# Optimization experiments

Measured on AMD Instinct MI355X. Metric: run time of the kernel, lower is better.

Reference implementation:

```python
import jax, jax.numpy as jnp
import numpy as np

T, B, V, LMAX = 512, 32, 4096, 32
NEG = -1e30  # log-domain 'zero'


def setup_inputs() -> dict:
    key = jax.random.key(0)
    k1, k2, k3, k4 = jax.random.split(key, 4)
    acts = jax.random.normal(k1, (T, B, V), dtype=jnp.float32)  # pre-softmax logits
    label_lens = jax.random.randint(k2, (B,), 16, LMAX + 1)
    act_lens = jax.random.randint(k3, (B,), T // 2, T + 1)
    total = int(jnp.sum(label_lens))
    labels = jax.random.randint(k4, (total,), 1, V)  # flat concat; blank=0 excluded
    return {"acts": acts, "labels": labels, "act_lens": act_lens, "label_lens": label_lens}


def _ctc_total_loss(acts, labels, act_lens, label_lens):
    # warp-ctc semantics: acts are logits; softmax applied internally; blank index = 0.
    logp = jax.nn.log_softmax(acts, axis=-1)  # (T, B, V)

    # Unpack flat concatenated labels into padded (B, LMAX).
    offsets = jnp.cumsum(label_lens) - label_lens
    pos = jnp.arange(LMAX)
    idx = jnp.clip(offsets[:, None] + pos[None, :], 0, labels.shape[0] - 1)
    lab = jnp.where(pos[None, :] < label_lens[:, None], labels[idx], 0)  # (B, LMAX)

    # Extended label sequence with interleaved blanks: S = 2*LMAX + 1.
    S = 2 * LMAX + 1
    ext = jnp.zeros((B, S), dtype=labels.dtype).at[:, 1::2].set(lab)
    s_idx = jnp.arange(S)
    s_valid = s_idx[None, :] < (2 * label_lens + 1)[:, None]  # (B, S)
    ext_m2 = jnp.concatenate([jnp.zeros((B, 2), ext.dtype), ext[:, :-2]], axis=1)
    can_skip = (ext != 0) & (ext != ext_m2) & (s_idx[None, :] >= 2)  # (B, S)

    # Pre-gather emissions along the lattice: (T, B, S).
    emit = jnp.take_along_axis(logp, ext[None, :, :], axis=2)

    alpha0 = jnp.where(s_idx[None, :] <= 1, emit[0], NEG)
    alpha0 = jnp.where(s_valid, alpha0, NEG)

    def step(alpha, xs):
        emit_t, t = xs
        a1 = jnp.concatenate([jnp.full((B, 1), NEG, alpha.dtype), alpha[:, :-1]], axis=1)
        a2 = jnp.concatenate([jnp.full((B, 2), NEG, alpha.dtype), alpha[:, :-2]], axis=1)
        a2 = jnp.where(can_skip, a2, NEG)
        m = jnp.maximum(alpha, jnp.maximum(a1, a2))
        new = m + jnp.log(jnp.exp(alpha - m) + jnp.exp(a1 - m) + jnp.exp(a2 - m)) + emit_t
        new = jnp.where(s_valid, new, NEG)
        # Freeze alpha once past each example's act_len (ragged time lengths).
        alpha = jnp.where((t < act_lens)[:, None], new, alpha)
        return alpha, None

    ts = jnp.arange(1, T)
    alpha, _ = jax.lax.scan(step, alpha0, (emit[1:], ts))

    end = 2 * label_lens  # final blank state per example
    l1 = jnp.take_along_axis(alpha, end[:, None], axis=1)[:, 0]
    l2 = jnp.take_along_axis(alpha, jnp.clip(end - 1, 0, S - 1)[:, None], axis=1)[:, 0]
    loss = -jnp.logaddexp(l1, l2)  # per-example NLL
    # size_average=False, length_average=False: return summed cost, shape (1,)
    return jnp.sum(loss)[None]


def reference(acts, labels, act_lens, label_lens):
    return _ctc_total_loss(acts, labels, act_lens, label_lens)
```

## Files before the change

### kernel.cpp

```cpp
#include <hip/hip_runtime.h>
#include <hip/hip_bf16.h>
#include <math.h>

#define T_DIM 512
#define B_DIM 32
#define V_DIM 4096
#define LMAX 32
#define S_DIM 65
#define NEG (-1e30f)
#define EROWS 528
#define LOG2E 1.4426950408889634f
#define LN2   0.6931471805599453f

__device__ __forceinline__ float fexp2(float x) {
#if __has_builtin(__builtin_amdgcn_exp2f)
    return __builtin_amdgcn_exp2f(x);
#else
    return exp2f(x);
#endif
}
__device__ __forceinline__ float flog2(float x) {
#if __has_builtin(__builtin_amdgcn_logf)
    return __builtin_amdgcn_logf(x);
#else
    return log2f(x);
#endif
}
__device__ __forceinline__ float gload(const float* p) {
    return *(const __attribute__((address_space(1))) float*)((unsigned long long)p);
}
__device__ __forceinline__ float lse2_2(float x, float y) {
    float m = fmaxf(x, y);
    return m + flog2(fexp2(x - m) + fexp2(y - m));
}
__device__ __forceinline__ float lse3_2(float x, float y, float z) {
    float m = fmaxf(x, fmaxf(y, z));
    return m + flog2(fexp2(x - m) + fexp2(y - m) + fexp2(z - m));
}

__global__ void k_ext(const int* __restrict__ labels,
                      const int* __restrict__ label_lens,
                      int total,
                      int* __restrict__ ext,
                      int* __restrict__ canskip) {
    int idx = blockIdx.x * blockDim.x + threadIdx.x;
    if (idx >= B_DIM * S_DIM) return;
    int b = idx / S_DIM;
    int s = idx % S_DIM;
    int off = 0;
    for (int i = 0; i < b; ++i) off += label_lens[i];
    int len = label_lens[b];

    auto getext = [&](int ss) -> int {
        if ((ss & 1) == 0) return 0;
        int j = ss >> 1;
        if (j >= len) return 0;
        int id = off + j;
        if (id > total - 1) id = total - 1;
        if (id < 0) id = 0;
        return labels[id];
    };

    int e = getext(s);
    ext[idx] = e;
    int cs = 0;
    if (s >= 2) {
        int em2 = getext(s - 2);
        cs = (e != 0 && e != em2) ? 1 : 0;
    }
    canskip[idx] = cs;
}

__global__ __launch_bounds__(256) void k_logz_emit(const float* __restrict__ acts,
                                                   const int* __restrict__ ext,
                                                   float* __restrict__ emitA,
                                                   float* __restrict__ emit64) {
    int bid = blockIdx.x;
    int t = bid / B_DIM;
    int b = bid % B_DIM;
    const float* row = acts + (size_t)bid * V_DIM;
    int tid = threadIdx.x;

    const float4* row4 = reinterpret_cast<const float4*>(row);
    float4 v[4];
#pragma unroll
    for (int k = 0; k < 4; ++k) v[k] = row4[tid + k * 256];

    float mx = -INFINITY;
#pragma unroll
    for (int k = 0; k < 4; ++k)
        mx = fmaxf(mx, fmaxf(fmaxf(v[k].x, v[k].y), fmaxf(v[k].z, v[k].w)));
#pragma unroll
    for (int off = 32; off > 0; off >>= 1) mx = fmaxf(mx, __shfl_xor(mx, off));

    __shared__ float smax[4], ssum[4];
    int wave = tid >> 6, lane = tid & 63;
    if (lane == 0) smax[wave] = mx;
    __syncthreads();
    mx = fmaxf(fmaxf(smax[0], smax[1]), fmaxf(smax[2], smax[3]));

    float mxL = mx * LOG2E;
    float s = 0.f;
#pragma unroll
    for (int k = 0; k < 4; ++k) {
        s += fexp2(fmaf(v[k].x, LOG2E, -mxL));
        s += fexp2(fmaf(v[k].y, LOG2E, -mxL));
        s += fexp2(fmaf(v[k].z, LOG2E, -mxL));
        s += fexp2(fmaf(v[k].w, LOG2E, -mxL));
    }
#pragma unroll
    for (int off = 32; off > 0; off >>= 1) s += __shfl_xor(s, off);
    if (lane == 0) ssum[wave] = s;
    __syncthreads();
    s = ssum[0] + ssum[1] + ssum[2] + ssum[3];

    float logZ2 = mxL + flog2(s);

    if (tid < 64) {
        int lab = ext[b * S_DIM + tid];
        emitA[((size_t)b * EROWS + t) * 64 + tid] = fmaf(row[lab], LOG2E, -logZ2);
    } else if (tid == 64) {
        emit64[(size_t)b * EROWS + t] = fmaf(row[0], LOG2E, -logZ2);
    }
}

__global__ __launch_bounds__(64) void k_forward(const float* __restrict__ emitA,
                                                const float* __restrict__ emit64,
                                                const int* __restrict__ canskip,
                                                const int* __restrict__ act_lens,
                                                const int* __restrict__ label_lens,
                                                float* __restrict__ losses) {
    int b = blockIdx.x;
    int l = threadIdx.x;
    int len = label_lens[b];
    int alen = act_lens[b];
    int Svalid = 2 * len + 1;
    bool validS  = l < Svalid;
    bool validM1 = (l >= 1) && (l - 1 < Svalid);
    bool validM2 = (l >= 2) && (l - 2 < Svalid);
    const int* csb = canskip + b * S_DIM;
    bool skipS  = csb[l] != 0;
    bool skipM1 = (l >= 1) ? (csb[l - 1] != 0) : false;
    bool skipM2 = (l >= 2) ? (csb[l - 2] != 0) : false;

    const float* pb  = emitA + (size_t)b * EROWS * 64;
    const float* p64 = emit64 + (size_t)b * EROWS;
    int lm1 = (l >= 1) ? l - 1 : 0;
    int lm2 = (l >= 2) ? l - 2 : 0;

    float a   = (l <= 1 && validS) ? gload(pb + l) : NEG;
    float a64 = NEG;

    float c0[4], cm1[4], cm2[4], c1[4], ca64[4], cb64[4];

#define LOADW(d0, dm1, dm2, d1, d64a, d64b, TB)                                 \
    _Pragma("unroll")                                                           \
    for (int r = 0; r < 4; ++r) {                                               \
        int tt = (TB) + 2 * r;                                                  \
        const float* rowp = pb + (size_t)tt * 64;                               \
        d0[r]   = gload(rowp + l);                                              \
        dm1[r]  = gload(rowp + lm1);                                            \
        dm2[r]  = gload(rowp + lm2);                                            \
        d1[r]   = gload(rowp + 64 + l);                                         \
        d64a[r] = gload(p64 + tt);                                              \
        d64b[r] = gload(p64 + tt + 1);                                          \
    }

    LOADW(c0, cm1, cm2, c1, ca64, cb64, 1)

    for (int w = 0; w < 64; ++w) {
        float n0[4], nm1[4], nm2[4], n1[4], na64[4], nb64[4];
        LOADW(n0, nm1, nm2, n1, na64, nb64, 1 + 8 * (w + 1))
#pragma unroll
        for (int r = 0; r < 4; ++r) {
            int t = 1 + 8 * w + 2 * r;
            float am1 = __shfl_up(a, 1); am1 = (l >= 1) ? am1 : NEG;
            float am2 = __shfl_up(a, 2); am2 = (l >= 2) ? am2 : NEG;
            float am3 = __shfl_up(a, 3); am3 = (l >= 3) ? am3 : NEG;
            float am4 = __shfl_up(a, 4); am4 = (l >= 4) ? am4 : NEG;
            float b0 = lse3_2(a,   am1, skipS  ? am2 : NEG) + c0[r];
            b0 = validS ? b0 : NEG;
            float b1 = lse3_2(am1, am2, skipM1 ? am3 : NEG) + cm1[r];
            b1 = validM1 ? b1 : NEG;
            float b2 = lse3_2(am2, am3, skipM2 ? am4 : NEG) + cm2[r];
            b2 = validM2 ? b2 : NEG;
            float cc = lse3_2(b0, b1, skipS ? b2 : NEG) + c1[r];
            cc = validS ? cc : NEG;
            float t64a = lse2_2(a64, a) + ca64[r];
            float t64b = lse2_2(t64a, b0) + cb64[r];
            bool r1 = t < alen, r2 = (t + 1) < alen;
            a   = r2 ? cc   : (r1 ? b0   : a);
            a64 = r2 ? t64b : (r1 ? t64a : a64);
        }
#pragma unroll
        for (int r = 0; r < 4; ++r) {
            c0[r] = n0[r]; cm1[r] = nm1[r]; cm2[r] = nm2[r]; c1[r] = n1[r];
            ca64[r] = na64[r]; cb64[r] = nb64[r];
        }
    }
#undef LOADW

    int end = 2 * len;
    float v64 = __shfl(a64, 63);
    float ae  = __shfl(a, end & 63);
    float l1 = (end == 64) ? v64 : ae;
    float l2 = __shfl(a, end - 1);
    float m = fmaxf(l1, l2);
    float loss = -LN2 * (m + flog2(fexp2(l1 - m) + fexp2(l2 - m)));
    if (l == 0) losses[b] = loss;
}

__global__ void k_sum(const float* __restrict__ losses, float* __restrict__ out) {
    int l = threadIdx.x;
    float v = (l < B_DIM) ? losses[l] : 0.f;
#pragma unroll
    for (int off = 32; off > 0; off >>= 1) v += __shfl_xor(v, off);
    if (l == 0) out[0] = v;
}

extern "C" void kernel_launch(void* const* d_in, const int* in_sizes, int n_in,
                              void* d_out, int out_size, void* d_ws, size_t ws_size,
                              hipStream_t stream) {
    const float* acts       = (const float*)d_in[0];
    const int*   labels     = (const int*)d_in[1];
    const int*   act_lens   = (const int*)d_in[2];
    const int*   label_lens = (const int*)d_in[3];
    int total_labels = in_sizes[1];

    char* ws = (char*)d_ws;
    int*   ext     = (int*)(ws);
    int*   canskip = (int*)(ws + 8320);
    float* losses  = (float*)(ws + 16640);
    float* emitA   = (float*)(ws + 16768);
    float* emit64  = (float*)(ws + 16768 + (size_t)B_DIM * EROWS * 64 * 4);
    float* out     = (float*)d_out;

    k_ext<<<(B_DIM * S_DIM + 255) / 256, 256, 0, stream>>>(labels, label_lens,
                                                           total_labels, ext, canskip);
    k_logz_emit<<<T_DIM * B_DIM, 256, 0, stream>>>(acts, ext, emitA, emit64);
    k_forward<<<B_DIM, 64, 0, stream>>>(emitA, emit64, canskip, act_lens,
                                        label_lens, losses);
    k_sum<<<1, 64, 0, stream>>>(losses, out);
}
```

Before: 431.6 us.

## Stage emission tiles into LDS with async global_load_lds double buffering

```diff
diff --git a/kernel.cpp b/kernel.cpp
--- a/kernel.cpp
+++ b/kernel.cpp
@@ -28,6 +28,16 @@
 }
 __device__ __forceinline__ float gload(const float* p) {
     return *(const __attribute__((address_space(1))) float*)((unsigned long long)p);
+}
+__device__ __forceinline__ void load_lds16(const float* g, float* l) {
+    __builtin_amdgcn_global_load_lds(
+        (const __attribute__((address_space(1))) unsigned int*)(const void*)g,
+        (__attribute__((address_space(3))) unsigned int*)(void*)l, 16, 0, 0);
+}
+__device__ __forceinline__ void load_lds4(const float* g, float* l) {
+    __builtin_amdgcn_global_load_lds(
+        (const __attribute__((address_space(1))) unsigned int*)(const void*)g,
+        (__attribute__((address_space(3))) unsigned int*)(void*)l, 4, 0, 0);
 }
 __device__ __forceinline__ float lse2_2(float x, float y) {
     float m = fmaxf(x, y);
@@ -130,6 +140,9 @@
                                                 const int* __restrict__ act_lens,
                                                 const int* __restrict__ label_lens,
                                                 float* __restrict__ losses) {
+    __shared__ float bufA[2][64 * 64];
+    __shared__ float buf64[2][64];
+
     int b = blockIdx.x;
     int l = threadIdx.x;
     int len = label_lens[b];
@@ -138,6 +151,7 @@
     bool validS  = l < Svalid;
     bool validM1 = (l >= 1) && (l - 1 < Svalid);
     bool validM2 = (l >= 2) && (l - 2 < Svalid);
+    bool has64 = (len == LMAX);
     const int* csb = canskip + b * S_DIM;
     bool skipS  = csb[l] != 0;
     bool skipM1 = (l >= 1) ? (csb[l - 1] != 0) : false;
@@ -148,57 +162,60 @@
     int lm1 = (l >= 1) ? l - 1 : 0;
     int lm2 = (l >= 2) ? l - 2 : 0;
 
-    float a   = (l <= 1 && validS) ? gload(pb + l) : NEG;
+    auto stage = [&](int g, int s) {
+        const float* gsrc = pb + (size_t)(64 * g + 1) * 64;
+#pragma unroll
+        for (int j = 0; j < 16; ++j)
+            load_lds16(gsrc + j * 256 + l * 4, &bufA[s][j * 256]);
+        if (has64)
+            load_lds4(p64 + 64 * g + 1 + l, &buf64[s][0]);
+    };
+
+    float a   = (l <= 1) ? gload(pb + l) : NEG;
     float a64 = NEG;
 
-    float c0[4], cm1[4], cm2[4], c1[4], ca64[4], cb64[4];
-
-#define LOADW(d0, dm1, dm2, d1, d64a, d64b, TB)                                 \
-    _Pragma("unroll")                                                           \
-    for (int r = 0; r < 4; ++r) {                                               \
-        int tt = (TB) + 2 * r;                                                  \
-        const float* rowp = pb + (size_t)tt * 64;                               \
-        d0[r]   = gload(rowp + l);                                              \
-        dm1[r]  = gload(rowp + lm1);                                            \
-        dm2[r]  = gload(rowp + lm2);                                            \
-        d1[r]   = gload(rowp + 64 + l);                                         \
-        d64a[r] = gload(p64 + tt);                                              \
-        d64b[r] = gload(p64 + tt + 1);                                          \
-    }
-
-    LOADW(c0, cm1, cm2, c1, ca64, cb64, 1)
-
-    for (int w = 0; w < 64; ++w) {
-        float n0[4], nm1[4], nm2[4], n1[4], na64[4], nb64[4];
-        LOADW(n0, nm1, nm2, n1, na64, nb64, 1 + 8 * (w + 1))
-#pragma unroll
-        for (int r = 0; r < 4; ++r) {
-            int t = 1 + 8 * w + 2 * r;
+    stage(0, 0);
+    asm volatile("s_waitcnt vmcnt(0)" ::: "memory");
+
+    for (int g = 0; g < 8; ++g) {
+        int cur = g & 1;
+        if (g < 7) stage(g + 1, cur ^ 1);
+
+#pragma unroll 4
+        for (int j = 0; j < 32; ++j) {
+            int t0 = 64 * g + 1 + 2 * j;
+            const float* base = &bufA[cur][2 * j * 64];
+            float c0  = base[l];
+            float cm1 = base[lm1];
+            float cm2 = base[lm2];
+            float c1  = base[64 + l];
+
             float am1 = __shfl_up(a, 1); am1 = (l >= 1) ? am1 : NEG;
             float am2 = __shfl_up(a, 2); am2 = (l >= 2) ? am2 : NEG;
             float am3 = __shfl_up(a, 3); am3 = (l >= 3) ? am3 : NEG;
             float am4 = __shfl_up(a, 4); am4 = (l >= 4) ? am4 : NEG;
-            float b0 = lse3_2(a,   am1, skipS  ? am2 : NEG) + c0[r];
+
+            float b0 = lse3_2(a,   am1, skipS  ? am2 : NEG) + c0;
             b0 = validS ? b0 : NEG;
-            float b1 = lse3_2(am1, am2, skipM1 ? am3 : NEG) + cm1[r];
+            float b1 = lse3_2(am1, am2, skipM1 ? am3 : NEG) + cm1;
             b1 = validM1 ? b1 : NEG;
-            float b2 = lse3_2(am2, am3, skipM2 ? am4 : NEG) + cm2[r];
+            float b2 = lse3_2(am2, am3, skipM2 ? am4 : NEG) + cm2;
             b2 = validM2 ? b2 : NEG;
-            float cc = lse3_2(b0, b1, skipS ? b2 : NEG) + c1[r];
+            float cc = lse3_2(b0, b1, skipS ? b2 : NEG) + c1;
             cc = validS ? cc : NEG;
-            float t64a = lse2_2(a64, a) + ca64[r];
-            float t64b = lse2_2(t64a, b0) + cb64[r];
-            bool r1 = t < alen, r2 = (t + 1) < alen;
-            a   = r2 ? cc   : (r1 ? b0   : a);
-            a64 = r2 ? t64b : (r1 ? t64a : a64);
+
+            bool r1 = t0 < alen, r2 = (t0 + 1) < alen;
+            if (has64) {
+                float ca64 = buf64[cur][2 * j];
+                float cb64 = buf64[cur][2 * j + 1];
+                float t64a = lse2_2(a64, a) + ca64;
+                float t64b = lse2_2(t64a, b0) + cb64;
+                a64 = r2 ? t64b : (r1 ? t64a : a64);
+            }
+            a = r2 ? cc : (r1 ? b0 : a);
         }
-#pragma unroll
-        for (int r = 0; r < 4; ++r) {
-            c0[r] = n0[r]; cm1[r] = nm1[r]; cm2[r] = nm2[r]; c1[r] = n1[r];
-            ca64[r] = na64[r]; cb64[r] = nb64[r];
-        }
-    }
-#undef LOADW
+        asm volatile("s_waitcnt vmcnt(0)" ::: "memory");
+    }
 
     int end = 2 * len;
     float v64 = __shfl(a64, 63);
```

Measured after the change: 434.6 us. No clear change (+0.7%).

## Map two lattice states per lane and step one time per iteration in CTC forward

Applied to the files above, without the earlier changes.

```diff
diff --git a/kernel.cpp b/kernel.cpp
--- a/kernel.cpp
+++ b/kernel.cpp
@@ -9,6 +9,7 @@
 #define S_DIM 65
 #define NEG (-1e30f)
 #define EROWS 528
+#define RSTRIDE 66
 #define LOG2E 1.4426950408889634f
 #define LN2   0.6931471805599453f
 
@@ -28,6 +29,13 @@
 }
 __device__ __forceinline__ float gload(const float* p) {
     return *(const __attribute__((address_space(1))) float*)((unsigned long long)p);
+}
+struct F2 { float x, y; };
+__device__ __forceinline__ F2 gload2(const float* p) {
+    F2 r;
+    r.x = gload(p);
+    r.y = gload(p + 1);
+    return r;
 }
 __device__ __forceinline__ float lse2_2(float x, float y) {
     float m = fmaxf(x, y);
@@ -73,8 +81,7 @@
 
 __global__ __launch_bounds__(256) void k_logz_emit(const float* __restrict__ acts,
                                                    const int* __restrict__ ext,
-                                                   float* __restrict__ emitA,
-                                                   float* __restrict__ emit64) {
+                                                   float* __restrict__ emitA) {
     int bid = blockIdx.x;
     int t = bid / B_DIM;
     int b = bid % B_DIM;
@@ -116,16 +123,13 @@
 
     float logZ2 = mxL + flog2(s);
 
-    if (tid < 64) {
+    if (tid < S_DIM) {
         int lab = ext[b * S_DIM + tid];
-        emitA[((size_t)b * EROWS + t) * 64 + tid] = fmaf(row[lab], LOG2E, -logZ2);
-    } else if (tid == 64) {
-        emit64[(size_t)b * EROWS + t] = fmaf(row[0], LOG2E, -logZ2);
+        emitA[((size_t)b * EROWS + t) * RSTRIDE + tid] = fmaf(row[lab], LOG2E, -logZ2);
     }
 }
 
 __global__ __launch_bounds__(64) void k_forward(const float* __restrict__ emitA,
-                                                const float* __restrict__ emit64,
                                                 const int* __restrict__ canskip,
                                                 const int* __restrict__ act_lens,
                                                 const int* __restrict__ label_lens,
@@ -135,76 +139,50 @@
     int len = label_lens[b];
     int alen = act_lens[b];
     int Svalid = 2 * len + 1;
-    bool validS  = l < Svalid;
-    bool validM1 = (l >= 1) && (l - 1 < Svalid);
-    bool validM2 = (l >= 2) && (l - 2 < Svalid);
+    int sH = 2 * l + 1;
+    bool validL = (2 * l) < Svalid;
+    bool validH = sH < Svalid;
     const int* csb = canskip + b * S_DIM;
-    bool skipS  = csb[l] != 0;
-    bool skipM1 = (l >= 1) ? (csb[l - 1] != 0) : false;
-    bool skipM2 = (l >= 2) ? (csb[l - 2] != 0) : false;
-
-    const float* pb  = emitA + (size_t)b * EROWS * 64;
-    const float* p64 = emit64 + (size_t)b * EROWS;
-    int lm1 = (l >= 1) ? l - 1 : 0;
-    int lm2 = (l >= 2) ? l - 2 : 0;
-
-    float a   = (l <= 1 && validS) ? gload(pb + l) : NEG;
-    float a64 = NEG;
-
-    float c0[4], cm1[4], cm2[4], c1[4], ca64[4], cb64[4];
-
-#define LOADW(d0, dm1, dm2, d1, d64a, d64b, TB)                                 \
-    _Pragma("unroll")                                                           \
-    for (int r = 0; r < 4; ++r) {                                               \
-        int tt = (TB) + 2 * r;                                                  \
-        const float* rowp = pb + (size_t)tt * 64;                               \
-        d0[r]   = gload(rowp + l);                                              \
-        dm1[r]  = gload(rowp + lm1);                                            \
-        dm2[r]  = gload(rowp + lm2);                                            \
-        d1[r]   = gload(rowp + 64 + l);                                         \
-        d64a[r] = gload(p64 + tt);                                              \
-        d64b[r] = gload(p64 + tt + 1);                                          \
-    }
-
-    LOADW(c0, cm1, cm2, c1, ca64, cb64, 1)
+    int csi = (sH < S_DIM) ? sH : (S_DIM - 1);
+    bool skipH = validH && (csb[csi] != 0);
+
+    const float* pb = emitA + (size_t)b * EROWS * RSTRIDE;
+
+    F2 e0 = gload2(pb + 2 * l);
+    float aL = (l == 0) ? e0.x : NEG;
+    float aH = (l == 0) ? e0.y : NEG;
+
+    F2 c[8];
+#pragma unroll
+    for (int j = 0; j < 8; ++j)
+        c[j] = gload2(pb + (size_t)(1 + j) * RSTRIDE + 2 * l);
 
     for (int w = 0; w < 64; ++w) {
-        float n0[4], nm1[4], nm2[4], n1[4], na64[4], nb64[4];
-        LOADW(n0, nm1, nm2, n1, na64, nb64, 1 + 8 * (w + 1))
-#pragma unroll
-        for (int r = 0; r < 4; ++r) {
-            int t = 1 + 8 * w + 2 * r;
-            float am1 = __shfl_up(a, 1); am1 = (l >= 1) ? am1 : NEG;
-            float am2 = __shfl_up(a, 2); am2 = (l >= 2) ? am2 : NEG;
-            float am3 = __shfl_up(a, 3); am3 = (l >= 3) ? am3 : NEG;
-            float am4 = __shfl_up(a, 4); am4 = (l >= 4) ? am4 : NEG;
-            float b0 = lse3_2(a,   am1, skipS  ? am2 : NEG) + c0[r];
-            b0 = validS ? b0 : NEG;
-            float b1 = lse3_2(am1, am2, skipM1 ? am3 : NEG) + cm1[r];
-            b1 = validM1 ? b1 : NEG;
-            float b2 = lse3_2(am2, am3, skipM2 ? am4 : NEG) + cm2[r];
-            b2 = validM2 ? b2 : NEG;
-            float cc = lse3_2(b0, b1, skipS ? b2 : NEG) + c1[r];
-            cc = validS ? cc : NEG;
-            float t64a = lse2_2(a64, a) + ca64[r];
-            float t64b = lse2_2(t64a, b0) + cb64[r];
-            bool r1 = t < alen, r2 = (t + 1) < alen;
-            a   = r2 ? cc   : (r1 ? b0   : a);
-            a64 = r2 ? t64b : (r1 ? t64a : a64);
+        F2 n[8];
+#pragma unroll
+        for (int j = 0; j < 8; ++j)
+            n[j] = gload2(pb + (size_t)(8 * (w + 1) + 1 + j) * RSTRIDE + 2 * l);
+
+#pragma unroll
+        for (int j = 0; j < 8; ++j) {
+            int t = 8 * w + 1 + j;
+            float pm1 = __shfl_up(aH, 1);
+            pm1 = (l >= 1) ? pm1 : NEG;
+            float nL = lse2_2(aL, pm1) + c[j].x;
+            nL = validL ? nL : NEG;
+            float nH = lse3_2(aH, aL, skipH ? pm1 : NEG) + c[j].y;
+            nH = validH ? nH : NEG;
+            bool run = t < alen;
+            aL = run ? nL : aL;
+            aH = run ? nH : aH;
         }
 #pragma unroll
-        for (int r = 0; r < 4; ++r) {
-            c0[r] = n0[r]; cm1[r] = nm1[r]; cm2[r] = nm2[r]; c1[r] = n1[r];
-            ca64[r] = na64[r]; cb64[r] = nb64[r];
-        }
-    }
-#undef LOADW
-
-    int end = 2 * len;
-    float v64 = __shfl(a64, 63);
-    float ae  = __shfl(a, end & 63);
-    float l1 = (end == 64) ? v64 : ae;
-    float l2 = __shfl(a, end - 1);
+        for (int j = 0; j < 8; ++j) c[j] = n[j];
+    }
+
+    int le = len;
+    float l1 = __shfl(aL, le);
+    float l2 = __shfl(aH, le - 1);
     float m = fmaxf(l1, l2);
     float loss = -LN2 * (m + flog2(fexp2(l1 - m) + fexp2(l2 - m)));
     if (l == 0) losses[b] = loss;
@@ -232,13 +210,12 @@
     int*   canskip = (int*)(ws + 8320);
     float* losses  = (float*)(ws + 16640);
     float* emitA   = (float*)(ws + 16768);
-    float* emit64  = (float*)(ws + 16768 + (size_t)B_DIM * EROWS * 64 * 4);
     float* out     = (float*)d_out;
 
     k_ext<<<(B_DIM * S_DIM + 255) / 256, 256, 0, stream>>>(labels, label_lens,
                                                            total_labels, ext, canskip);
-    k_logz_emit<<<T_DIM * B_DIM, 256, 0, stream>>>(acts, ext, emitA, emit64);
-    k_forward<<<B_DIM, 64, 0, stream>>>(emitA, emit64, canskip, act_lens,
+    k_logz_emit<<<T_DIM * B_DIM, 256, 0, stream>>>(acts, ext, emitA);
+    k_forward<<<B_DIM, 64, 0, stream>>>(emitA, canskip, act_lens,
                                         label_lens, losses);
     k_sum<<<1, 64, 0, stream>>>(losses, out);
 }
```

Result: faster. 418.7 us (-3.0%).
